# Performance work log

Measured on AMD Instinct MI355X. Metric: run time of the kernel, lower is better.

Reference implementation:

```python
import jax, jax.numpy as jnp
import numpy as np

N, E, G, H, L = 50000, 800000, 512, 128, 3
NF, EF = 128, 16
EPS = 1e-5


def _bn(x, g, b):
    # BatchNorm1d in training mode: biased batch statistics over dim 0
    mu = x.mean(0)
    var = x.var(0)
    return g * (x - mu) * jax.lax.rsqrt(var + EPS) + b


def setup_inputs() -> dict:
    key = jax.random.key(0)
    ks = jax.random.split(key, 16)
    s = 0.05
    return {
        "x": jax.random.normal(ks[0], (N, NF), jnp.float32),
        "edge_attr": jax.random.normal(ks[1], (E, EF), jnp.float32),
        "atom_W": jax.random.normal(ks[2], (NF, H), jnp.float32) * s,
        "atom_b": jnp.zeros((H,), jnp.float32),
        "vn_emb": jax.random.normal(ks[3], (H,), jnp.float32) * s,
        "conv_We": jax.random.normal(ks[4], (L, EF, H), jnp.float32) * s,
        "conv_be": jnp.zeros((L, H), jnp.float32),
        "conv_W": jax.random.normal(ks[5], (L, H, H), jnp.float32) * s,
        "conv_b": jnp.zeros((L, H), jnp.float32),
        "conv_g": jnp.ones((L, H), jnp.float32),
        "conv_beta": jnp.zeros((L, H), jnp.float32),
        "vn1_W": jax.random.normal(ks[6], (L, 2 * H, 2 * H), jnp.float32) * s,
        "vn1_b": jnp.zeros((L, 2 * H), jnp.float32),
        "vn1_g": jnp.ones((L, 2 * H), jnp.float32),
        "vn1_beta": jnp.zeros((L, 2 * H), jnp.float32),
        "vn2_W": jax.random.normal(ks[7], (L, 2 * H, H), jnp.float32) * s,
        "vn2_b": jnp.zeros((L, H), jnp.float32),
        "vn2_g": jnp.ones((L, H), jnp.float32),
        "vn2_beta": jnp.zeros((L, H), jnp.float32),
        "pred_W1": jax.random.normal(ks[8], (L * H, L * H), jnp.float32) * s,
        "pred_b1": jnp.zeros((L * H,), jnp.float32),
        "pred_W2": jax.random.normal(ks[9], (L * H, 1), jnp.float32) * s,
        "pred_b2": jnp.zeros((1,), jnp.float32),
        "edge_index": jax.random.randint(ks[10], (2, E), 0, N),
        "batch": jnp.sort(jax.random.randint(ks[11], (N,), 0, G)),
    }


def reference(x, edge_attr, atom_W, atom_b, vn_emb, conv_We, conv_be, conv_W,
              conv_b, conv_g, conv_beta, vn1_W, vn1_b, vn1_g, vn1_beta,
              vn2_W, vn2_b, vn2_g, vn2_beta, pred_W1, pred_b1, pred_W2,
              pred_b2, edge_index, batch):
    src, dst = edge_index[0], edge_index[1]
    h = x @ atom_W + atom_b                      # atom_encoder: [N, H]
    vn = jnp.broadcast_to(vn_emb, (G, H))        # virtual node per graph
    vxs = []
    for i in range(L):
        h = h + vn[batch]                         # gather virtual node by graph id
        # CombConv: edge-conditioned GIN-style message passing
        e = edge_attr @ conv_We[i] + conv_be[i]   # [E, H]
        msg = jax.nn.relu(h[src] + e)             # gather + fuse
        agg = jax.ops.segment_sum(msg, dst, num_segments=N)
        h = jax.nn.relu(_bn((h + agg) @ conv_W[i] + conv_b[i], conv_g[i], conv_beta[i]))
        # virtual node update: gather -> MLP1 -> segment pool -> MLP2
        t = jnp.concatenate([vn[batch], h], axis=-1)          # [N, 2H]
        t = jax.nn.relu(_bn(t @ vn1_W[i] + vn1_b[i], vn1_g[i], vn1_beta[i]))
        pooled = jax.ops.segment_sum(t, batch, num_segments=G)  # global_add_pool
        vn = jax.nn.relu(_bn(pooled @ vn2_W[i] + vn2_b[i], vn2_g[i], vn2_beta[i]))
        vxs.append(vn)
    hg = jnp.concatenate(vxs, axis=-1)            # JK='C': [G, L*H]
    hg = jax.nn.relu(hg @ pred_W1 + pred_b1)
    return hg @ pred_W2 + pred_b2                 # [G, 1]
```

## Files before the change

kernel.cpp:

```cpp
#include <hip/hip_runtime.h>
#include <hip/hip_fp16.h>

constexpr int N = 50000;
constexpr int E = 800000;
constexpr int G = 512;
constexpr int H = 128;
constexpr long long NH = (long long)N * H;
constexpr float EPS = 1e-5f;
constexpr int NB_SCAN = 196;

typedef _Float16 f16x8 __attribute__((ext_vector_type(8)));
typedef _Float16 f16x2 __attribute__((ext_vector_type(2)));
typedef float f32x4 __attribute__((ext_vector_type(4)));

__global__ void k_init_vn(const float* __restrict__ vn_emb, float* __restrict__ vn) {
  int idx = blockIdx.x * 256 + threadIdx.x;
  vn[idx] = vn_emb[idx & 127];
}

__global__ void k_tof16(const float* __restrict__ in, __half* __restrict__ out, int n4) {
  int i = blockIdx.x * 256 + threadIdx.x;
  if (i >= n4) return;
  float4 v = reinterpret_cast<const float4*>(in)[i];
  __half2* o = reinterpret_cast<__half2*>(out);
  o[i * 2]     = __floats2half2_rn(v.x, v.y);
  o[i * 2 + 1] = __floats2half2_rn(v.z, v.w);
}

__global__ void k_wt(const float* __restrict__ W, __half* __restrict__ Wt,
                     int ldw, int row0, int cols, long long wstride, int wtstride) {
  const float* Wl = W + (long long)blockIdx.y * wstride;
  __half* Wtl = Wt + (long long)blockIdx.y * wtstride;
  int idx = blockIdx.x * 256 + threadIdx.x;
  int k = idx & 127, c = idx >> 7;
  Wtl[c * 128 + k] = __float2half(Wl[(long long)(row0 + k) * ldw + c]);
}

__global__ void k_addvn16(__half* __restrict__ h16, const float* __restrict__ vn,
                          const int* __restrict__ batch) {
  int i2 = blockIdx.x * 256 + threadIdx.x;
  int r = i2 >> 6;
  int b = batch[r];
  __half2 hv = reinterpret_cast<__half2*>(h16)[i2];
  float2 vv = reinterpret_cast<const float2*>(vn)[(b << 6) + (i2 & 63)];
  reinterpret_cast<__half2*>(h16)[i2] =
      __floats2half2_rn(__low2float(hv) + vv.x, __high2float(hv) + vv.y);
}

__global__ void k_gstart(const int* __restrict__ batch, int* __restrict__ gstart) {
  int g = threadIdx.x;
  int lo = 0, hi = N;
  while (lo < hi) { int mid = (lo + hi) >> 1; if (batch[mid] < g) lo = mid + 1; else hi = mid; }
  gstart[g] = lo;
  if (g == 0) gstart[G] = N;
}

__global__ void k_hist(const int* __restrict__ dst, int* __restrict__ cnt) {
  int e = blockIdx.x * 256 + threadIdx.x;
  atomicAdd(&cnt[dst[e]], 1);
}

__global__ void k_scan_block(const int* __restrict__ cnt, int* __restrict__ off,
                             int* __restrict__ bsum) {
  __shared__ int s[256];
  int idx = blockIdx.x * 256 + threadIdx.x;
  int v = (idx < N) ? cnt[idx] : 0;
  s[threadIdx.x] = v;
  __syncthreads();
  for (int o = 1; o < 256; o <<= 1) {
    int t = (threadIdx.x >= o) ? s[threadIdx.x - o] : 0;
    __syncthreads();
    s[threadIdx.x] += t;
    __syncthreads();
  }
  if (idx < N) off[idx + 1] = s[threadIdx.x];
  if (threadIdx.x == 255) bsum[blockIdx.x] = s[255];
  if (idx == 0) off[0] = 0;
}

__global__ void k_scan_bsum(int* __restrict__ bsum) {
  __shared__ int s[256];
  int v = (threadIdx.x < NB_SCAN) ? bsum[threadIdx.x] : 0;
  s[threadIdx.x] = v;
  __syncthreads();
  for (int o = 1; o < 256; o <<= 1) {
    int t = (threadIdx.x >= o) ? s[threadIdx.x - o] : 0;
    __syncthreads();
    s[threadIdx.x] += t;
    __syncthreads();
  }
  if (threadIdx.x < NB_SCAN) bsum[threadIdx.x] = s[threadIdx.x];
}

__global__ void k_scan_add(int* __restrict__ off, const int* __restrict__ bsum) {
  int idx = blockIdx.x * 256 + threadIdx.x;
  if (idx < N && blockIdx.x > 0) off[idx + 1] += bsum[blockIdx.x - 1];
}

__global__ void k_scatter_idx(const int* __restrict__ dst, const int* __restrict__ off,
                              int* __restrict__ cur, int* __restrict__ eidp) {
  int e = blockIdx.x * 256 + threadIdx.x;
  int d = dst[e];
  int p = off[d] + atomicAdd(&cur[d], 1);
  eidp[p] = e;
}

__global__ void k_permute(const int* __restrict__ eidp, const int* __restrict__ src,
                          const float* __restrict__ edge_attr,
                          int* __restrict__ srcp, __half* __restrict__ eap) {
  int i = blockIdx.x * 256 + threadIdx.x;
  int e = eidp[i];
  srcp[i] = src[e] * 64;
  const float4* ea4 = reinterpret_cast<const float4*>(edge_attr) + e * 4;
  float4 a0 = ea4[0], a1 = ea4[1], a2 = ea4[2], a3 = ea4[3];
  __half2 h01 = __floats2half2_rn(a0.x, a0.y);
  __half2 h23 = __floats2half2_rn(a0.z, a0.w);
  __half2 h45 = __floats2half2_rn(a1.x, a1.y);
  __half2 h67 = __floats2half2_rn(a1.z, a1.w);
  __half2 h89 = __floats2half2_rn(a2.x, a2.y);
  __half2 hab = __floats2half2_rn(a2.z, a2.w);
  __half2 hcd = __floats2half2_rn(a3.x, a3.y);
  __half2 hef = __floats2half2_rn(a3.z, a3.w);
  int4 lo = make_int4(__builtin_bit_cast(int, h01), __builtin_bit_cast(int, h23),
                      __builtin_bit_cast(int, h45), __builtin_bit_cast(int, h67));
  int4 hi = make_int4(__builtin_bit_cast(int, h89), __builtin_bit_cast(int, hab),
                      __builtin_bit_cast(int, hcd), __builtin_bit_cast(int, hef));
  int4* o = reinterpret_cast<int4*>(eap + (long long)i * 16);
  o[0] = lo;
  o[1] = hi;
}

__global__ __launch_bounds__(256) void k_agg(
    const __half* __restrict__ eap, const float* __restrict__ We,
    const float* __restrict__ be, const int* __restrict__ off,
    const int* __restrict__ srcp, const __half* __restrict__ h16,
    __half* __restrict__ hpa16, int d0) {
  int tid = threadIdx.x;
  int lane = tid & 63;
  int c0 = lane * 2;
  f16x2 wc0[8], wc1[8];
#pragma unroll
  for (int kk = 0; kk < 8; ++kk) {
    f16x2 w0, w1;
    w0[0] = (_Float16)We[(2 * kk) * 128 + c0];
    w0[1] = (_Float16)We[(2 * kk + 1) * 128 + c0];
    w1[0] = (_Float16)We[(2 * kk) * 128 + c0 + 1];
    w1[1] = (_Float16)We[(2 * kk + 1) * 128 + c0 + 1];
    wc0[kk] = w0; wc1[kk] = w1;
  }
  float2 bev = reinterpret_cast<const float2*>(be)[lane];
  int d = d0 + blockIdx.x * 4 + (tid >> 6);
  int j0 = off[d], j1 = off[d + 1];
  const __half2* h2 = reinterpret_cast<const __half2*>(h16);
  const int4* e4 = reinterpret_cast<const int4*>(eap);
  float a0 = 0.f, a1 = 0.f, b0 = 0.f, b1 = 0.f;
  float p0 = 0.f, p1 = 0.f, q0 = 0.f, q1 = 0.f;
  int j = j0;
#define EDGE(J, A0, A1) do {                                                   \
    int s_ = srcp[(J)];                                                        \
    __half2 hv_ = h2[s_ + lane];                                               \
    int4 lo_ = e4[2 * (J)], hi_ = e4[2 * (J) + 1];                             \
    float ev0_ = bev.x, ev1_ = bev.y;                                          \
    ev0_ = __builtin_amdgcn_fdot2(__builtin_bit_cast(f16x2, lo_.x), wc0[0], ev0_, false); \
    ev1_ = __builtin_amdgcn_fdot2(__builtin_bit_cast(f16x2, lo_.x), wc1[0], ev1_, false); \
    ev0_ = __builtin_amdgcn_fdot2(__builtin_bit_cast(f16x2, lo_.y), wc0[1], ev0_, false); \
    ev1_ = __builtin_amdgcn_fdot2(__builtin_bit_cast(f16x2, lo_.y), wc1[1], ev1_, false); \
    ev0_ = __builtin_amdgcn_fdot2(__builtin_bit_cast(f16x2, lo_.z), wc0[2], ev0_, false); \
    ev1_ = __builtin_amdgcn_fdot2(__builtin_bit_cast(f16x2, lo_.z), wc1[2], ev1_, false); \
    ev0_ = __builtin_amdgcn_fdot2(__builtin_bit_cast(f16x2, lo_.w), wc0[3], ev0_, false); \
    ev1_ = __builtin_amdgcn_fdot2(__builtin_bit_cast(f16x2, lo_.w), wc1[3], ev1_, false); \
    ev0_ = __builtin_amdgcn_fdot2(__builtin_bit_cast(f16x2, hi_.x), wc0[4], ev0_, false); \
    ev1_ = __builtin_amdgcn_fdot2(__builtin_bit_cast(f16x2, hi_.x), wc1[4], ev1_, false); \
    ev0_ = __builtin_amdgcn_fdot2(__builtin_bit_cast(f16x2, hi_.y), wc0[5], ev0_, false); \
    ev1_ = __builtin_amdgcn_fdot2(__builtin_bit_cast(f16x2, hi_.y), wc1[5], ev1_, false); \
    ev0_ = __builtin_amdgcn_fdot2(__builtin_bit_cast(f16x2, hi_.z), wc0[6], ev0_, false); \
    ev1_ = __builtin_amdgcn_fdot2(__builtin_bit_cast(f16x2, hi_.z), wc1[6], ev1_, false); \
    ev0_ = __builtin_amdgcn_fdot2(__builtin_bit_cast(f16x2, hi_.w), wc0[7], ev0_, false); \
    ev1_ = __builtin_amdgcn_fdot2(__builtin_bit_cast(f16x2, hi_.w), wc1[7], ev1_, false); \
    A0 += fmaxf(__low2float(hv_) + ev0_, 0.f);                                 \
    A1 += fmaxf(__high2float(hv_) + ev1_, 0.f);                                \
  } while (0)
  for (; j + 3 < j1; j += 4) {
    EDGE(j, a0, a1);
    EDGE(j + 1, b0, b1);
    EDGE(j + 2, p0, p1);
    EDGE(j + 3, q0, q1);
  }
  for (; j < j1; ++j) EDGE(j, a0, a1);
#undef EDGE
  a0 += b0 + p0 + q0; a1 += b1 + p1 + q1;
  int di = d * 64 + lane;
  __half2 hd = h2[di];
  reinterpret_cast<__half2*>(hpa16)[di] =
      __floats2half2_rn(__low2float(hd) + a0, __high2float(hd) + a1);
}

template<bool HAS_BIAS, bool HAS_ROWBIAS, bool OUT_F16, bool STATS>
__global__ __launch_bounds__(256) void k_mgemm(
    const __half* __restrict__ A, const __half* __restrict__ Bt,
    const float* __restrict__ bias, const float* __restrict__ bias2,
    const float* __restrict__ rowbias, const int* __restrict__ batch,
    float* __restrict__ Cf, __half* __restrict__ Ch,
    float* __restrict__ stats, int ldc, int M) {
  __shared__ _Float16 Bsh[128][136];
  int tid = threadIdx.x;
  int m0 = blockIdx.x * 64;
  int c0 = blockIdx.y * 128;
  int wid = tid >> 6, lane = tid & 63;
  int wr = wid >> 1, wc = wid & 1;
  int lrow = lane & 15;
  int lk = (lane >> 4) * 8;

  f16x8 af[4][2];
#pragma unroll
  for (int kk = 0; kk < 4; ++kk)
#pragma unroll
    for (int fm = 0; fm < 2; ++fm)
      af[kk][fm] = *reinterpret_cast<const f16x8*>(
          A + (m0 + wr * 32 + fm * 16 + lrow) * 128 + kk * 32 + lk);

#pragma unroll
  for (int it = 0; it < 8; ++it) {
    int idx = it * 256 + tid;
    int r = idx >> 4, ck = idx & 15;
    f16x8 v = *reinterpret_cast<const f16x8*>(Bt + ((c0 + r) << 7) + ck * 8);
    *reinterpret_cast<f16x8*>(&Bsh[r][ck * 8]) = v;
  }
  __syncthreads();

  f32x4 acc[2][4];
#pragma unroll
  for (int fm = 0; fm < 2; ++fm)
#pragma unroll
    for (int fn = 0; fn < 4; ++fn) acc[fm][fn] = (f32x4){0.f, 0.f, 0.f, 0.f};

#pragma unroll
  for (int kk = 0; kk < 4; ++kk) {
    f16x8 bf[4];
#pragma unroll
    for (int fn = 0; fn < 4; ++fn)
      bf[fn] = *reinterpret_cast<const f16x8*>(&Bsh[wc * 64 + fn * 16 + lrow][kk * 32 + lk]);
#pragma unroll
    for (int fm = 0; fm < 2; ++fm)
#pragma unroll
      for (int fn = 0; fn < 4; ++fn)
        acc[fm][fn] = __builtin_amdgcn_mfma_f32_16x16x32_f16(af[kk][fm], bf[fn], acc[fm][fn], 0, 0, 0);
  }

  float ss[4], ss2[4];
#pragma unroll
  for (int fn = 0; fn < 4; ++fn) { ss[fn] = 0.f; ss2[fn] = 0.f; }
#pragma unroll
  for (int fn = 0; fn < 4; ++fn) {
    int col = c0 + wc * 64 + fn * 16 + lrow;
    float bb = HAS_BIAS ? bias[col] : 0.f;
    if (HAS_BIAS && bias2 != nullptr) bb += bias2[col];
#pragma unroll
    for (int fm = 0; fm < 2; ++fm) {
      int grb = m0 + wr * 32 + fm * 16 + (lane >> 4) * 4;
#pragma unroll
      for (int j = 0; j < 4; ++j) {
        int gr = grb + j;
        if (gr < M) {
          float v = acc[fm][fn][j] + bb;
          if (HAS_ROWBIAS)
            v += rowbias[batch[gr] * ldc + col];
          if (STATS) { ss[fn] += v; ss2[fn] += v * v; }
          if (OUT_F16)
            Ch[(long long)gr * ldc + col] = __float2half(v);
          else
            Cf[(long long)gr * ldc + col] = v;
        }
      }
    }
  }
  if (STATS) {
    __shared__ float sred[2][4][4][16];
#pragma unroll
    for (int fn = 0; fn < 4; ++fn) {
      float s = ss[fn], s2 = ss2[fn];
      s += __shfl_xor(s, 16);  s += __shfl_xor(s, 32);
      s2 += __shfl_xor(s2, 16); s2 += __shfl_xor(s2, 32);
      if (lane < 16) { sred[0][wid][fn][lane] = s; sred[1][wid][fn][lane] = s2; }
    }
    __syncthreads();
    if (wr == 0 && lane < 16) {
#pragma unroll
      for (int fn = 0; fn < 4; ++fn) {
        int col = c0 + wc * 64 + fn * 16 + lane;
        atomicAdd(&stats[col],       sred[0][wid][fn][lane] + sred[0][wid + 2][fn][lane]);
        atomicAdd(&stats[ldc + col], sred[1][wid][fn][lane] + sred[1][wid + 2][fn][lane]);
      }
    }
  }
}

template<int K, bool HAS_BIAS, bool HAS_ROWBIAS, bool RELU, bool STATS>
__global__ __launch_bounds__(256) void k_gemm(
    const float* __restrict__ A1,
    const float* __restrict__ W, int ldw,
    const float* __restrict__ bias,
    const float* __restrict__ rowbias, const int* __restrict__ batch,
    float* __restrict__ C, float* __restrict__ stats, int M) {
  __shared__ float As[32 * K];
  constexpr int K4 = K / 4;
  int tid = threadIdx.x;
  int m0 = blockIdx.x * 32;
#pragma unroll
  for (int it = 0; it < K / 32; ++it) {
    int e4 = it * 256 + tid;
    int r = e4 / K4;
    int k4 = e4 % K4;
    int gr = m0 + r;
    float4 v = make_float4(0.f, 0.f, 0.f, 0.f);
    if (gr < M) v = reinterpret_cast<const float4*>(A1)[(long long)gr * K4 + k4];
    reinterpret_cast<float4*>(As)[e4] = v;
  }
  __shared__ float cs[128], cs2[128];
  if (STATS && tid < 128) { cs[tid] = 0.f; cs2[tid] = 0.f; }
  __syncthreads();

  int cg = tid & 31;
  int rg = tid >> 5;
  int col = blockIdx.y * 128 + cg * 4;
  float4 acc[4];
#pragma unroll
  for (int j = 0; j < 4; ++j) acc[j] = make_float4(0.f, 0.f, 0.f, 0.f);
  const float4* W4 = reinterpret_cast<const float4*>(W);
  const float4* As4 = reinterpret_cast<const float4*>(As);
#pragma unroll 8
  for (int k = 0; k < K; k += 4) {
    float4 w0 = W4[((k + 0) * ldw + col) >> 2];
    float4 w1 = W4[((k + 1) * ldw + col) >> 2];
    float4 w2 = W4[((k + 2) * ldw + col) >> 2];
    float4 w3 = W4[((k + 3) * ldw + col) >> 2];
#pragma unroll
    for (int j = 0; j < 4; ++j) {
      float4 a = As4[(rg + j * 8) * K4 + (k >> 2)];
      acc[j].x += a.x * w0.x + a.y * w1.x + a.z * w2.x + a.w * w3.x;
      acc[j].y += a.x * w0.y + a.y * w1.y + a.z * w2.y + a.w * w3.y;
      acc[j].z += a.x * w0.z + a.y * w1.z + a.z * w2.z + a.w * w3.z;
      acc[j].w += a.x * w0.w + a.y * w1.w + a.z * w2.w + a.w * w3.w;
    }
  }
  float4 bb = make_float4(0.f, 0.f, 0.f, 0.f);
  if (HAS_BIAS) bb = reinterpret_cast<const float4*>(bias)[blockIdx.y * 32 + cg];
  float ps[4] = {0.f, 0.f, 0.f, 0.f}, ps2[4] = {0.f, 0.f, 0.f, 0.f};
#pragma unroll
  for (int j = 0; j < 4; ++j) {
    int gr = m0 + rg + j * 8;
    if (gr < M) {
      float4 v = acc[j];
      v.x += bb.x; v.y += bb.y; v.z += bb.z; v.w += bb.w;
      if (HAS_ROWBIAS) {
        int b = batch[gr];
        float4 rb = reinterpret_cast<const float4*>(rowbias)[((long long)b * ldw + col) >> 2];
        v.x += rb.x; v.y += rb.y; v.z += rb.z; v.w += rb.w;
      }
      if (RELU) {
        v.x = fmaxf(v.x, 0.f); v.y = fmaxf(v.y, 0.f);
        v.z = fmaxf(v.z, 0.f); v.w = fmaxf(v.w, 0.f);
      }
      if (STATS) {
        ps[0] += v.x; ps2[0] += v.x * v.x;
        ps[1] += v.y; ps2[1] += v.y * v.y;
        ps[2] += v.z; ps2[2] += v.z * v.z;
        ps[3] += v.w; ps2[3] += v.w * v.w;
      }
      reinterpret_cast<float4*>(C)[((long long)gr * ldw + col) >> 2] = v;
    }
  }
  if (STATS) {
#pragma unroll
    for (int jc = 0; jc < 4; ++jc) {
      atomicAdd(&cs[cg * 4 + jc], ps[jc]);
      atomicAdd(&cs2[cg * 4 + jc], ps2[jc]);
    }
    __syncthreads();
    if (tid < 128) {
      atomicAdd(&stats[blockIdx.y * 128 + tid], cs[tid]);
      atomicAdd(&stats[ldw + blockIdx.y * 128 + tid], cs2[tid]);
    }
  }
}

__global__ void k_bn16(const __half* __restrict__ X16, const float* __restrict__ stats,
                       const float* __restrict__ gam, const float* __restrict__ beta,
                       __half* __restrict__ out16, float invM) {
  int i2 = blockIdx.x * 256 + threadIdx.x;
  int c = (i2 & 63) * 2;
  __half2 xv = reinterpret_cast<const __half2*>(X16)[i2];
  float m0 = stats[c] * invM;
  float v0 = stats[128 + c] * invM - m0 * m0;
  float m1 = stats[c + 1] * invM;
  float v1 = stats[128 + c + 1] * invM - m1 * m1;
  float r0 = fmaxf((__low2float(xv) - m0) * rsqrtf(v0 + EPS) * gam[c] + beta[c], 0.f);
  float r1 = fmaxf((__high2float(xv) - m1) * rsqrtf(v1 + EPS) * gam[c + 1] + beta[c + 1], 0.f);
  reinterpret_cast<__half2*>(out16)[i2] = __floats2half2_rn(r0, r1);
}

__global__ void k_pool(const __half* __restrict__ z2_16, const float* __restrict__ stats,
                       const float* __restrict__ gam, const float* __restrict__ beta,
                       const int* __restrict__ gstart, float* __restrict__ pooled) {
  int tid = threadIdx.x;
  int rsub = tid >> 7;
  int cl = tid & 127;
  int g = blockIdx.x;
  int c = blockIdx.y * 128 + cl;
  const float invM = 1.f / (float)N;
  float mean = stats[c] * invM;
  float var = stats[256 + c] * invM - mean * mean;
  float scale = rsqrtf(var + EPS) * gam[c];
  float shift = beta[c] - mean * scale;
  int r0 = gstart[g], r1 = gstart[g + 1];
  float acc = 0.f;
  for (int r = r0 + rsub; r < r1; r += 4) {
    float v = __half2float(z2_16[(long long)r * 256 + c]);
    acc += fmaxf(v * scale + shift, 0.f);
  }
  __shared__ float sred[512];
  sred[tid] = acc;
  __syncthreads();
  if (rsub == 0)
    pooled[g * 256 + c] = sred[cl] + sred[128 + cl] + sred[256 + cl] + sred[384 + cl];
}

__global__ void k_vnapply(const float* __restrict__ zvn, const float* __restrict__ stats,
                          const float* __restrict__ gam, const float* __restrict__ beta,
                          float* __restrict__ vn, float* __restrict__ hgbuf, int layer) {
  int idx = blockIdx.x * 256 + threadIdx.x;
  int c = idx & 127;
  int g = idx >> 7;
  const float invM = 1.f / (float)G;
  float mean = stats[c] * invM;
  float var = stats[128 + c] * invM - mean * mean;
  float v = fmaxf((zvn[idx] - mean) * rsqrtf(var + EPS) * gam[c] + beta[c], 0.f);
  vn[idx] = v;
  hgbuf[g * 384 + layer * 128 + c] = v;
}

__global__ void k_pred2(const float* __restrict__ hg2, const float* __restrict__ W2,
                        const float* __restrict__ b2, float* __restrict__ out) {
  int g = blockIdx.x;
  int lane = threadIdx.x;
  float s = 0.f;
  for (int k = lane; k < 384; k += 64) s += hg2[g * 384 + k] * W2[k];
  for (int off = 32; off; off >>= 1) s += __shfl_down(s, off);
  if (lane == 0) out[g] = s + b2[0];
}

extern "C" void kernel_launch(void* const* d_in, const int* in_sizes, int n_in,
                              void* d_out, int out_size, void* d_ws, size_t ws_size,
                              hipStream_t stream) {
  const float* x         = (const float*)d_in[0];
  const float* edge_attr = (const float*)d_in[1];
  const float* atom_W    = (const float*)d_in[2];
  const float* atom_b    = (const float*)d_in[3];
  const float* vn_emb    = (const float*)d_in[4];
  const float* conv_We   = (const float*)d_in[5];
  const float* conv_be   = (const float*)d_in[6];
  const float* conv_W    = (const float*)d_in[7];
  const float* conv_b    = (const float*)d_in[8];
  const float* conv_g    = (const float*)d_in[9];
  const float* conv_beta = (const float*)d_in[10];
  const float* vn1_W     = (const float*)d_in[11];
  const float* vn1_b     = (const float*)d_in[12];
  const float* vn1_g     = (const float*)d_in[13];
  const float* vn1_beta  = (const float*)d_in[14];
  const float* vn2_W     = (const float*)d_in[15];
  const float* vn2_b     = (const float*)d_in[16];
  const float* vn2_g     = (const float*)d_in[17];
  const float* vn2_beta  = (const float*)d_in[18];
  const float* pred_W1   = (const float*)d_in[19];
  const float* pred_b1   = (const float*)d_in[20];
  const float* pred_W2   = (const float*)d_in[21];
  const float* pred_b2   = (const float*)d_in[22];
  const int*   eidx      = (const int*)d_in[23];
  const int*   batch     = (const int*)d_in[24];
  const int* src = eidx;
  const int* dst = eidx + E;

  float* ws    = (float*)d_ws;
  __half* h16  = (__half*)ws;
  float* bufB  = ws + NH / 2;
  __half* hpa16= (__half*)bufB;
  __half* z16  = (__half*)(bufB + NH / 2);
  __half* x16  = z16;
  __half* z2_16= (__half*)(bufB + NH);
  float* smallz= bufB + 2 * NH;
  float* U     = smallz;
  float* pooled= U + G * 256;
  float* zvn   = pooled + G * 256;
  float* vn    = zvn + G * 128;
  float* hgbuf = vn + G * 128;
  float* hg2   = hgbuf + G * 384;
  float* statsz= hg2 + G * 384;
  int*   gstart= (int*)(statsz + 3 * 1024);
  __half* atomWt = (__half*)(gstart + 516);
  __half* convWt = atomWt + 16384;
  __half* z2Wt   = convWt + 3 * 16384;
  int*  off    = (int*)(z2Wt + 3 * 32768);
  int*  srcp   = off + 50002;
  __half* eap  = (__half*)(srcp + E);
  int* cnt  = (int*)bufB;
  int* cur  = cnt + N;
  int* bsum = cur + N;
  int* eidp = cur + N + 256;

  dim3 b256(256);

  hipMemsetAsync(cnt, 0, (size_t)(2 * N + NB_SCAN) * 4, stream);
  hipMemsetAsync(statsz, 0, 3 * 1024 * 4, stream);
  k_hist<<<E / 256, b256, 0, stream>>>(dst, cnt);
  k_scan_block<<<NB_SCAN, b256, 0, stream>>>(cnt, off, bsum);
  k_scan_bsum<<<1, b256, 0, stream>>>(bsum);
  k_scan_add<<<NB_SCAN, b256, 0, stream>>>(off, bsum);
  k_scatter_idx<<<E / 256, b256, 0, stream>>>(dst, off, cur, eidp);
  k_permute<<<E / 256, b256, 0, stream>>>(eidp, src, edge_attr, srcp, eap);
  k_gstart<<<1, G, 0, stream>>>(batch, gstart);

  k_init_vn<<<G * 128 / 256, b256, 0, stream>>>(vn_emb, vn);

  k_tof16<<<(N * 128 / 4 + 255) / 256, b256, 0, stream>>>(x, x16, N * 128 / 4);
  k_wt<<<dim3(64, 1), b256, 0, stream>>>(atom_W, atomWt, 128, 0, 128, 0, 0);
  k_wt<<<dim3(64, 3), b256, 0, stream>>>(conv_W, convWt, 128, 0, 128, 16384, 16384);
  k_wt<<<dim3(128, 3), b256, 0, stream>>>(vn1_W, z2Wt, 256, 128, 256, 65536, 32768);

  k_mgemm<true, false, true, false><<<dim3(782, 1), b256, 0, stream>>>(
      x16, atomWt, atom_b, vn_emb, nullptr, nullptr, nullptr, h16, nullptr, 128, N);

  for (int i = 0; i < 3; ++i) {
    float* SZ = statsz + i * 1024;
    if (i > 0) k_addvn16<<<12500, b256, 0, stream>>>(h16, vn, batch);
    k_agg<<<6250, b256, 0, stream>>>(eap, conv_We + i * 2048, conv_be + i * 128,
                                     off, srcp, h16, hpa16, 0);
    k_agg<<<6250, b256, 0, stream>>>(eap, conv_We + i * 2048, conv_be + i * 128,
                                     off, srcp, h16, hpa16, 25000);
    k_mgemm<true, false, true, true><<<dim3(782, 1), b256, 0, stream>>>(
        hpa16, convWt + i * 16384, conv_b + i * 128, nullptr, nullptr, nullptr,
        nullptr, z16, SZ, 128, N);
    k_bn16<<<12500, b256, 0, stream>>>(z16, SZ, conv_g + i * 128, conv_beta + i * 128,
                                       h16, 1.f / (float)N);
    k_gemm<128, true, false, false, false><<<dim3(16, 2), b256, 0, stream>>>(
        vn, vn1_W + i * 256 * 256, 256, vn1_b + i * 256, nullptr, nullptr, U, nullptr, G);
    k_mgemm<false, true, true, true><<<dim3(782, 2), b256, 0, stream>>>(
        h16, z2Wt + i * 32768, nullptr, nullptr, U, batch, nullptr, z2_16,
        SZ + 256, 256, N);
    k_pool<<<dim3(G, 2), dim3(512), 0, stream>>>(
        z2_16, SZ + 256, vn1_g + i * 256, vn1_beta + i * 256, gstart, pooled);
    k_gemm<256, true, false, false, true><<<dim3(16, 1), b256, 0, stream>>>(
        pooled, vn2_W + i * 256 * 128, 128, vn2_b + i * 128, nullptr, nullptr,
        zvn, SZ + 768, G);
    k_vnapply<<<G * 128 / 256, b256, 0, stream>>>(
        zvn, SZ + 768, vn2_g + i * 128, vn2_beta + i * 128, vn, hgbuf, i);
  }
  k_gemm<384, true, false, true, false><<<dim3(16, 3), b256, 0, stream>>>(
      hgbuf, pred_W1, 384, pred_b1, nullptr, nullptr, hg2, nullptr, G);
  k_pred2<<<G, 64, 0, stream>>>(hg2, pred_W2, pred_b2, (float*)d_out);
}
```

Before: 1.210 ms.

## Split-K the small virtual-node and prediction GEMMs with atomic accumulation

Replaces the small fp32 GEMM kernel with a split-K variant that spreads K over four z-blocks and accumulates into zero-initialised outputs with atomics. Stats and ReLU can no longer sit in its epilogue, so BN statistics move to a separate k_stats kernel and the prediction ReLU moves into k_pred2. Buffers are reordered so that U and zvn are contiguous and one memset per layer clears both. The aim is to raise parallelism for these latency-bound GEMMs (only 16-48 blocks before), at the cost of extra memsets, an extra stats launch and atomic traffic.

```diff
diff --git a/kernel.cpp b/kernel.cpp
--- a/kernel.cpp
+++ b/kernel.cpp
@@ -295,29 +295,22 @@
   }
 }
 
-template<int K, bool HAS_BIAS, bool HAS_ROWBIAS, bool RELU, bool STATS>
-__global__ __launch_bounds__(256) void k_gemm(
-    const float* __restrict__ A1,
+template<int KC, bool HAS_BIAS>
+__global__ __launch_bounds__(256) void k_sgemm(
+    const float* __restrict__ A1, int lda,
     const float* __restrict__ W, int ldw,
     const float* __restrict__ bias,
-    const float* __restrict__ rowbias, const int* __restrict__ batch,
-    float* __restrict__ C, float* __restrict__ stats, int M) {
-  __shared__ float As[32 * K];
-  constexpr int K4 = K / 4;
+    float* __restrict__ C) {
+  __shared__ float As[32 * KC];
+  constexpr int K4 = KC / 4;
   int tid = threadIdx.x;
   int m0 = blockIdx.x * 32;
-#pragma unroll
-  for (int it = 0; it < K / 32; ++it) {
-    int e4 = it * 256 + tid;
-    int r = e4 / K4;
-    int k4 = e4 % K4;
-    int gr = m0 + r;
-    float4 v = make_float4(0.f, 0.f, 0.f, 0.f);
-    if (gr < M) v = reinterpret_cast<const float4*>(A1)[(long long)gr * K4 + k4];
-    reinterpret_cast<float4*>(As)[e4] = v;
-  }
-  __shared__ float cs[128], cs2[128];
-  if (STATS && tid < 128) { cs[tid] = 0.f; cs2[tid] = 0.f; }
+  int kbase = blockIdx.z * KC;
+  for (int e4 = tid; e4 < 32 * K4; e4 += 256) {
+    int r = e4 / K4, k4 = e4 % K4;
+    reinterpret_cast<float4*>(As)[e4] = *reinterpret_cast<const float4*>(
+        &A1[(long long)(m0 + r) * lda + kbase + k4 * 4]);
+  }
   __syncthreads();
 
   int cg = tid & 31;
@@ -328,12 +321,12 @@
   for (int j = 0; j < 4; ++j) acc[j] = make_float4(0.f, 0.f, 0.f, 0.f);
   const float4* W4 = reinterpret_cast<const float4*>(W);
   const float4* As4 = reinterpret_cast<const float4*>(As);
-#pragma unroll 8
-  for (int k = 0; k < K; k += 4) {
-    float4 w0 = W4[((k + 0) * ldw + col) >> 2];
-    float4 w1 = W4[((k + 1) * ldw + col) >> 2];
-    float4 w2 = W4[((k + 2) * ldw + col) >> 2];
-    float4 w3 = W4[((k + 3) * ldw + col) >> 2];
+#pragma unroll 4
+  for (int k = 0; k < KC; k += 4) {
+    float4 w0 = W4[((kbase + k + 0) * ldw + col) >> 2];
+    float4 w1 = W4[((kbase + k + 1) * ldw + col) >> 2];
+    float4 w2 = W4[((kbase + k + 2) * ldw + col) >> 2];
+    float4 w3 = W4[((kbase + k + 3) * ldw + col) >> 2];
 #pragma unroll
     for (int j = 0; j < 4; ++j) {
       float4 a = As4[(rg + j * 8) * K4 + (k >> 2)];
@@ -344,44 +337,39 @@
     }
   }
   float4 bb = make_float4(0.f, 0.f, 0.f, 0.f);
-  if (HAS_BIAS) bb = reinterpret_cast<const float4*>(bias)[blockIdx.y * 32 + cg];
-  float ps[4] = {0.f, 0.f, 0.f, 0.f}, ps2[4] = {0.f, 0.f, 0.f, 0.f};
+  if (HAS_BIAS && blockIdx.z == 0)
+    bb = reinterpret_cast<const float4*>(bias)[blockIdx.y * 32 + cg];
 #pragma unroll
   for (int j = 0; j < 4; ++j) {
     int gr = m0 + rg + j * 8;
-    if (gr < M) {
-      float4 v = acc[j];
-      v.x += bb.x; v.y += bb.y; v.z += bb.z; v.w += bb.w;
-      if (HAS_ROWBIAS) {
-        int b = batch[gr];
-        float4 rb = reinterpret_cast<const float4*>(rowbias)[((long long)b * ldw + col) >> 2];
-        v.x += rb.x; v.y += rb.y; v.z += rb.z; v.w += rb.w;
-      }
-      if (RELU) {
-        v.x = fmaxf(v.x, 0.f); v.y = fmaxf(v.y, 0.f);
-        v.z = fmaxf(v.z, 0.f); v.w = fmaxf(v.w, 0.f);
-      }
-      if (STATS) {
-        ps[0] += v.x; ps2[0] += v.x * v.x;
-        ps[1] += v.y; ps2[1] += v.y * v.y;
-        ps[2] += v.z; ps2[2] += v.z * v.z;
-        ps[3] += v.w; ps2[3] += v.w * v.w;
-      }
-      reinterpret_cast<float4*>(C)[((long long)gr * ldw + col) >> 2] = v;
+    float* cp = &C[(long long)gr * ldw + col];
+    atomicAdd(cp + 0, acc[j].x + bb.x);
+    atomicAdd(cp + 1, acc[j].y + bb.y);
+    atomicAdd(cp + 2, acc[j].z + bb.z);
+    atomicAdd(cp + 3, acc[j].w + bb.w);
+  }
+}
+
+template<int NC>
+__global__ void k_stats(const float* __restrict__ X, int M, float* __restrict__ stats) {
+  constexpr int RP = 256 / NC;
+  int c = threadIdx.x % NC;
+  int rsub = threadIdx.x / NC;
+  float s = 0.f, s2 = 0.f;
+  for (int r = blockIdx.x * RP + rsub; r < M; r += gridDim.x * RP) {
+    float v = X[(long long)r * NC + c];
+    s += v; s2 += v * v;
+  }
+  if (RP > 1) {
+    __shared__ float ls[512];
+    ls[threadIdx.x] = s; ls[256 + threadIdx.x] = s2;
+    __syncthreads();
+    if (rsub == 0) {
+#pragma unroll
+      for (int j = 1; j < RP; ++j) { s += ls[j * NC + c]; s2 += ls[256 + j * NC + c]; }
     }
   }
-  if (STATS) {
-#pragma unroll
-    for (int jc = 0; jc < 4; ++jc) {
-      atomicAdd(&cs[cg * 4 + jc], ps[jc]);
-      atomicAdd(&cs2[cg * 4 + jc], ps2[jc]);
-    }
-    __syncthreads();
-    if (tid < 128) {
-      atomicAdd(&stats[blockIdx.y * 128 + tid], cs[tid]);
-      atomicAdd(&stats[ldw + blockIdx.y * 128 + tid], cs2[tid]);
-    }
-  }
+  if (rsub == 0) { atomicAdd(&stats[c], s); atomicAdd(&stats[NC + c], s2); }
 }
 
 __global__ void k_bn16(const __half* __restrict__ X16, const float* __restrict__ stats,
@@ -444,7 +432,7 @@
   int g = blockIdx.x;
   int lane = threadIdx.x;
   float s = 0.f;
-  for (int k = lane; k < 384; k += 64) s += hg2[g * 384 + k] * W2[k];
+  for (int k = lane; k < 384; k += 64) s += fmaxf(hg2[g * 384 + k], 0.f) * W2[k];
   for (int off = 32; off; off >>= 1) s += __shfl_down(s, off);
   if (lane == 0) out[g] = s + b2[0];
 }
@@ -489,9 +477,9 @@
   __half* z2_16= (__half*)(bufB + NH);
   float* smallz= bufB + 2 * NH;
   float* U     = smallz;
-  float* pooled= U + G * 256;
-  float* zvn   = pooled + G * 256;
-  float* vn    = zvn + G * 128;
+  float* zvn   = U + G * 256;
+  float* pooled= zvn + G * 128;
+  float* vn    = pooled + G * 256;
   float* hgbuf = vn + G * 128;
   float* hg2   = hgbuf + G * 384;
   float* statsz= hg2 + G * 384;
@@ -531,6 +519,7 @@
 
   for (int i = 0; i < 3; ++i) {
     float* SZ = statsz + i * 1024;
+    hipMemsetAsync(U, 0, (size_t)G * (256 + 128) * 4, stream);
     if (i > 0) k_addvn16<<<12500, b256, 0, stream>>>(h16, vn, batch);
     k_agg<<<6250, b256, 0, stream>>>(eap, conv_We + i * 2048, conv_be + i * 128,
                                      off, srcp, h16, hpa16, 0);
@@ -541,20 +530,21 @@
         nullptr, z16, SZ, 128, N);
     k_bn16<<<12500, b256, 0, stream>>>(z16, SZ, conv_g + i * 128, conv_beta + i * 128,
                                        h16, 1.f / (float)N);
-    k_gemm<128, true, false, false, false><<<dim3(16, 2), b256, 0, stream>>>(
-        vn, vn1_W + i * 256 * 256, 256, vn1_b + i * 256, nullptr, nullptr, U, nullptr, G);
+    k_sgemm<32, true><<<dim3(16, 2, 4), b256, 0, stream>>>(
+        vn, 128, vn1_W + i * 256 * 256, 256, vn1_b + i * 256, U);
     k_mgemm<false, true, true, true><<<dim3(782, 2), b256, 0, stream>>>(
         h16, z2Wt + i * 32768, nullptr, nullptr, U, batch, nullptr, z2_16,
         SZ + 256, 256, N);
     k_pool<<<dim3(G, 2), dim3(512), 0, stream>>>(
         z2_16, SZ + 256, vn1_g + i * 256, vn1_beta + i * 256, gstart, pooled);
-    k_gemm<256, true, false, false, true><<<dim3(16, 1), b256, 0, stream>>>(
-        pooled, vn2_W + i * 256 * 128, 128, vn2_b + i * 128, nullptr, nullptr,
-        zvn, SZ + 768, G);
+    k_sgemm<64, true><<<dim3(16, 1, 4), b256, 0, stream>>>(
+        pooled, 256, vn2_W + i * 256 * 128, 128, vn2_b + i * 128, zvn);
+    k_stats<128><<<16, b256, 0, stream>>>(zvn, G, SZ + 768);
     k_vnapply<<<G * 128 / 256, b256, 0, stream>>>(
         zvn, SZ + 768, vn2_g + i * 128, vn2_beta + i * 128, vn, hgbuf, i);
   }
-  k_gemm<384, true, false, true, false><<<dim3(16, 3), b256, 0, stream>>>(
-      hgbuf, pred_W1, 384, pred_b1, nullptr, nullptr, hg2, nullptr, G);
+  hipMemsetAsync(hg2, 0, (size_t)G * 384 * 4, stream);
+  k_sgemm<96, true><<<dim3(16, 3, 4), b256, 0, stream>>>(
+      hgbuf, 384, pred_W1, 384, pred_b1, hg2);
   k_pred2<<<G, 64, 0, stream>>>(hg2, pred_W2, pred_b2, (float*)d_out);
 }
```

Result: faster. 1.098 ms (-9.2%).
